# Kernel tuning notes

Measured on AMD Instinct MI355X. Metric: run time of the kernel, lower is better.

The kernel has to match this reference:

```python
import jax, jax.numpy as jnp
import numpy as np

N_NODES, N_EDGES, D_IN, D_H, N_GRAPHS = 50000, 600000, 1024, 128, 1000


def _transformer_conv(x, src, dst, wq, bq, wk, bk, wv, bv, ws, bs, n):
    """PyG TransformerConv, heads=1, concat=True, root_weight=True."""
    q = x @ wq + bq                      # [N, d]
    k = x @ wk + bk
    v = x @ wv + bv
    d = q.shape[-1]
    # per-edge attention score for edge j->i: <q_i, k_j> / sqrt(d)
    score = jnp.sum(q[dst] * k[src], axis=-1) / jnp.sqrt(jnp.asarray(d, x.dtype))  # [E]
    # segment softmax over incoming edges of each destination node
    smax = jax.ops.segment_max(score, dst, num_segments=n)
    smax = jnp.where(jnp.isfinite(smax), smax, jnp.zeros_like(smax))
    ex = jnp.exp(score - smax[dst])
    denom = jax.ops.segment_sum(ex, dst, num_segments=n)
    alpha = ex / (denom[dst] + 1e-16)
    # scatter-aggregate weighted values back to destination nodes
    agg = jax.ops.segment_sum(alpha[:, None] * v[src], dst, num_segments=n)  # [N, d]
    # skip (root) connection
    return agg + x @ ws + bs


def setup_inputs() -> dict:
    key = jax.random.key(0)
    ks = jax.random.split(key, 20)
    inp = {}
    inp['x'] = jax.random.normal(ks[0], (N_NODES, D_IN), dtype=jnp.float32)
    inp['edge_index'] = jax.random.randint(ks[1], (2, N_EDGES), 0, N_NODES, dtype=jnp.int64)
    inp['idx'] = jax.random.randint(ks[2], (N_GRAPHS,), 0, N_NODES, dtype=jnp.int64)
    s_in = 0.02
    # layer 0: 1024 -> 128
    for i, nm in enumerate(['wq0', 'wk0', 'wv0', 'ws0']):
        inp[nm] = jax.random.normal(ks[3 + i], (D_IN, D_H), dtype=jnp.float32) * s_in
    for nm in ['bq0', 'bk0', 'bv0', 'bs0']:
        inp[nm] = jnp.zeros((D_H,), dtype=jnp.float32)
    # layer 1: 128 -> 128
    for i, nm in enumerate(['wq1', 'wk1', 'wv1', 'ws1']):
        inp[nm] = jax.random.normal(ks[7 + i], (D_H, D_H), dtype=jnp.float32) * 0.08
    for nm in ['bq1', 'bk1', 'bv1', 'bs1']:
        inp[nm] = jnp.zeros((D_H,), dtype=jnp.float32)
    # MLP head 128 -> 128 -> 64 -> 1
    inp['mw1'] = jax.random.normal(ks[11], (D_H, D_H), dtype=jnp.float32) * 0.08
    inp['mb1'] = jnp.zeros((D_H,), dtype=jnp.float32)
    inp['mw2'] = jax.random.normal(ks[12], (D_H, 64), dtype=jnp.float32) * 0.08
    inp['mb2'] = jnp.zeros((64,), dtype=jnp.float32)
    inp['mw3'] = jax.random.normal(ks[13], (64, 1), dtype=jnp.float32) * 0.1
    inp['mb3'] = jnp.zeros((1,), dtype=jnp.float32)
    return inp


def reference(x, edge_index, idx,
              wq0, bq0, wk0, bk0, wv0, bv0, ws0, bs0,
              wq1, bq1, wk1, bk1, wv1, bv1, ws1, bs1,
              mw1, mb1, mw2, mb2, mw3, mb3):
    src, dst = edge_index[0], edge_index[1]
    n = x.shape[0]
    h = _transformer_conv(x, src, dst, wq0, bq0, wk0, bk0, wv0, bv0, ws0, bs0, n)
    h = jax.nn.relu(h)
    h = _transformer_conv(h, src, dst, wq1, bq1, wk1, bk1, wv1, bv1, ws1, bs1, n)
    h = jax.nn.relu(h)
    h = h[idx]                           # one center node per graph -> [B, d]
    h = jax.nn.relu(h @ mw1 + mb1)       # dropout is identity in eval
    h = jax.nn.relu(h @ mw2 + mb2)
    out = jax.nn.sigmoid(h @ mw3 + mb3)  # [B, 1]
    return out
```

## Files before the change

### kernel.cpp

```cpp
#include <hip/hip_runtime.h>
#include <hip/hip_bf16.h>
#include <cstdint>
#include <cstddef>

typedef __bf16 bf16x2 __attribute__((ext_vector_type(2)));
typedef __bf16 bf16x8 __attribute__((ext_vector_type(8)));
typedef float f32x4 __attribute__((ext_vector_type(4)));

__device__ __forceinline__ void gl_lds16(const __bf16* g, __bf16* l) {
    __builtin_amdgcn_global_load_lds(
        (const __attribute__((address_space(1))) unsigned int*)g,
        (__attribute__((address_space(3))) unsigned int*)l, 16, 0, 0);
}

template <typename AT> struct ARaw;
template <> struct ARaw<float>  { float4 u, v; };
template <> struct ARaw<__bf16> { bf16x8 w; };

template <typename AT>
__device__ __forceinline__ void loadAraw(const AT* p, ARaw<AT>& r) {
    if constexpr (sizeof(AT) == 4) {
        r.u = *(const float4*)p;
        r.v = *(const float4*)(p + 4);
    } else {
        r.w = *(const bf16x8*)p;
    }
}

template <typename AT>
__device__ __forceinline__ bf16x8 cvtA(const ARaw<AT>& r) {
    if constexpr (sizeof(AT) == 4) {
        return (bf16x8){(__bf16)r.u.x, (__bf16)r.u.y, (__bf16)r.u.z, (__bf16)r.u.w,
                        (__bf16)r.v.x, (__bf16)r.v.y, (__bf16)r.v.z, (__bf16)r.v.w};
    } else {
        return r.w;
    }
}

__global__ __launch_bounds__(256) void mark_idx_kernel(const int* __restrict__ idx,
                                                       int* __restrict__ flagIdx,
                                                       int* __restrict__ flagU, int B) {
    int t = blockIdx.x * 256 + threadIdx.x;
    if (t < B) {
        int n = idx[t];
        flagIdx[n] = 1;
        flagU[n] = 1;
    }
}

__global__ __launch_bounds__(256) void hist_mark_kernel(const int* __restrict__ esrc,
                                                        const int* __restrict__ edst,
                                                        const int* __restrict__ flagIdx,
                                                        int* __restrict__ deg,
                                                        int* __restrict__ flagU, int E) {
    int e = blockIdx.x * 256 + threadIdx.x;
    if (e < E) {
        int d = edst[e];
        atomicAdd(&deg[d], 1);
        if (flagIdx[d]) flagU[esrc[e]] = 1;
    }
}

__global__ __launch_bounds__(1024) void scan8_kernel(const int* __restrict__ deg,
                                                     int* __restrict__ off, int n,
                                                     const int* __restrict__ flagU,
                                                     int* __restrict__ U,
                                                     int* __restrict__ nU) {
    __shared__ int wsum[16];
    int tid = threadIdx.x, lane = tid & 63, wid = tid >> 6;
    if (tid == 0) off[0] = 0;
    int carry = 0;
    int nchunk = (n + 8191) >> 13;
    for (int c = 0; c < nchunk; ++c) {
        int base = (c << 13) + tid * 8;
        int4 a = *(const int4*)(deg + base);
        int4 b = *(const int4*)(deg + base + 4);
        int s[8];
        s[0] = a.x; s[1] = s[0] + a.y; s[2] = s[1] + a.z; s[3] = s[2] + a.w;
        s[4] = s[3] + b.x; s[5] = s[4] + b.y; s[6] = s[5] + b.z; s[7] = s[6] + b.w;
        int x = s[7];
        for (int o = 1; o < 64; o <<= 1) {
            int t = __shfl_up(x, o, 64);
            if (lane >= o) x += t;
        }
        if (lane == 63) wsum[wid] = x;
        __syncthreads();
        if (wid == 0 && lane < 16) {
            int w = wsum[lane];
            for (int o = 1; o < 16; o <<= 1) {
                int t = __shfl_up(w, o, 64);
                if (lane >= o) w += t;
            }
            wsum[lane] = w;
        }
        __syncthreads();
        int pre = carry + (wid ? wsum[wid - 1] : 0) + (x - s[7]);
#pragma unroll
        for (int i = 0; i < 8; ++i)
            if (base + i < n) off[base + i + 1] = pre + s[i];
        carry += wsum[15];
        __syncthreads();
    }
    for (int i = tid; i < n; i += 1024)
        if (flagU[i]) U[atomicAdd(nU, 1)] = i;
}

__global__ __launch_bounds__(256) void scatter_kernel(const int* __restrict__ src,
                                                      const int* __restrict__ dst,
                                                      const int* __restrict__ off,
                                                      int* __restrict__ cursor,
                                                      int* __restrict__ srcs, int E) {
    int e = blockIdx.x * 256 + threadIdx.x;
    if (e < E) {
        int d = dst[e];
        int p = off[d] + atomicAdd(&cursor[d], 1);
        srcs[p] = src[e];
    }
}

__global__ __launch_bounds__(256) void pack_w_kernel(const float* __restrict__ wq0, const float* __restrict__ wk0,
                                                     const float* __restrict__ wv0, const float* __restrict__ ws0,
                                                     const float* __restrict__ wq1, const float* __restrict__ wk1,
                                                     const float* __restrict__ wv1, const float* __restrict__ ws1,
                                                     const float* __restrict__ bq0, const float* __restrict__ bk0,
                                                     const float* __restrict__ bv0, const float* __restrict__ bs0,
                                                     const float* __restrict__ bq1, const float* __restrict__ bk1,
                                                     const float* __restrict__ bv1, const float* __restrict__ bs1,
                                                     __bf16* __restrict__ w0t, __bf16* __restrict__ w1t,
                                                     float* __restrict__ b0, float* __restrict__ b1) {
    int i = blockIdx.x * 256 + threadIdx.x;
    const int S0 = 512 * 1024, S1 = 512 * 128;
    if (i < S0) {
        int n = i >> 10, k = i & 1023;
        int sel = n >> 7, c = n & 127;
        const float* w = (sel == 0) ? wk0 : (sel == 1) ? wv0 : (sel == 2) ? wq0 : ws0;
        w0t[i] = (__bf16)w[(size_t)k * 128 + c];
    } else if (i < S0 + S1) {
        int j = i - S0;
        int n = j >> 7, k = j & 127;
        int sel = n >> 7, c = n & 127;
        const float* w = (sel == 0) ? wk1 : (sel == 1) ? wv1 : (sel == 2) ? wq1 : ws1;
        w1t[j] = (__bf16)w[(size_t)k * 128 + c];
    } else if (i < S0 + S1 + 512) {
        int t = i - S0 - S1;
        int sel = t >> 7, c = t & 127;
        const float* b = (sel == 0) ? bk0 : (sel == 1) ? bv0 : (sel == 2) ? bq0 : bs0;
        b0[t] = b[c];
    } else if (i < S0 + S1 + 1024) {
        int t = i - S0 - S1 - 512;
        int sel = t >> 7, c = t & 127;
        const float* b = (sel == 0) ? bk1 : (sel == 1) ? bv1 : (sel == 2) ? bq1 : bs1;
        b1[t] = b[c];
    }
}

template <typename AT>
__global__ __launch_bounds__(512, 4) void gemm_dual_kernel(const AT* __restrict__ A,
                                                           const __bf16* __restrict__ Bt,
                                                           const float* __restrict__ bias,
                                                           __bf16* __restrict__ outb,
                                                           float* __restrict__ outf,
                                                           const int* __restrict__ rl0,
                                                           const int* __restrict__ np0, int ns0,
                                                           const int* __restrict__ rl1,
                                                           const int* __restrict__ np1, int ns1,
                                                           int K, int s0blocks) {
    __shared__ __align__(16) __bf16 Asl[2][128 * 32];
    __shared__ __align__(16) __bf16 Bsl[3][256 * 32];
    const int bx = blockIdx.x;
    const int sector = (bx >= s0blocks) ? 1 : 0;
    const int tile0  = sector ? bx - s0blocks : bx;
    const int tstr   = sector ? (gridDim.x - s0blocks) : s0blocks;
    const int* rowlist = sector ? rl1 : rl0;
    const int* nptr = sector ? np1 : np0;
    const int nrows = nptr ? *nptr : (sector ? ns1 : ns0);
    if (nrows <= 0) return;
    const __bf16* BT = Bt + (size_t)(sector ? 256 : 0) * K;
    const float* bs = bias + (sector ? 256 : 0);
    const int ntiles = (nrows + 127) >> 7;
    const int NT = K >> 5;

    const int tid = threadIdx.x;
    const int lane = tid & 63, wid = tid >> 6;
    const int wm = wid >> 2, wn = wid & 3;
    const int fr = lane & 15, quad = lane >> 4;
    const int rr = tid >> 2;
    const int kc8 = (tid & 3) << 3;
    const int swch = (((tid & 3) ^ (rr & 3)) << 3);
    const int qsw8 = ((quad ^ (fr & 3)) << 3);

    const __bf16* gB = BT + (size_t)rr * K + swch;

    for (int mt = tile0; mt < ntiles; mt += tstr) {
        const int mbase = mt << 7;
        int lr = mbase + rr;
        if (lr >= nrows) lr = nrows - 1;
        const int gr = rowlist ? rowlist[lr] : lr;
        const AT* gA = A + (size_t)gr * K + kc8;

        f32x4 acc[4][4];
#pragma unroll
        for (int i = 0; i < 4; i++)
#pragma unroll
            for (int j = 0; j < 4; j++) acc[i][j] = (f32x4){0.f, 0.f, 0.f, 0.f};

        __syncthreads();

        ARaw<AT> a0, aC;
        {
            __bf16* bd0 = &Bsl[0][(size_t)(wid << 4) * 32];
            gl_lds16(gB, bd0);
            gl_lds16(gB + (size_t)128 * K, bd0 + 128 * 32);
            loadAraw(gA, a0);
            __bf16* bd1 = &Bsl[1][(size_t)(wid << 4) * 32];
            gl_lds16(gB + 32, bd1);
            gl_lds16(gB + (size_t)128 * K + 32, bd1 + 128 * 32);
            loadAraw(gA + 32, aC);
            *(bf16x8*)&Asl[0][rr * 32 + swch] = cvtA<AT>(a0);
            asm volatile("s_waitcnt lgkmcnt(0)" ::: "memory");
            __builtin_amdgcn_s_barrier();
        }

        for (int k = 0; k < NT; ++k) {
            const __bf16* As = Asl[k & 1];
            const __bf16* Bs = Bsl[k % 3];
            bf16x8 af[4];
#pragma unroll
            for (int mi = 0; mi < 4; mi++)
                af[mi] = *(const bf16x8*)&As[(wm * 64 + mi * 16 + fr) * 32 + qsw8];
#pragma unroll
            for (int ni = 0; ni < 4; ni++) {
                bf16x8 b8 = *(const bf16x8*)&Bs[(wn * 64 + ni * 16 + fr) * 32 + qsw8];
#pragma unroll
                for (int mi = 0; mi < 4; mi++)
                    acc[mi][ni] = __builtin_amdgcn_mfma_f32_16x16x32_bf16(af[mi], b8, acc[mi][ni], 0, 0, 0);
            }
            const bool wr = (k + 1 < NT);
            const bool pf = (k + 2 < NT);
            if (pf) {
                const int kn = (k + 2) << 5;
                __bf16* bd = &Bsl[(k + 2) % 3][(size_t)(wid << 4) * 32];
                gl_lds16(gB + kn, bd);
                gl_lds16(gB + (size_t)128 * K + kn, bd + 128 * 32);
            }
            if (wr) {
                *(bf16x8*)&Asl[(k + 1) & 1][rr * 32 + swch] = cvtA<AT>(aC);
            }
            if (pf) {
                loadAraw(gA + ((k + 2) << 5), aC);
            }
            if (wr) {
                asm volatile("s_waitcnt lgkmcnt(0)" ::: "memory");
                __builtin_amdgcn_s_barrier();
            }
        }

#pragma unroll
        for (int mi = 0; mi < 4; mi++)
#pragma unroll
            for (int ni = 0; ni < 4; ni++) {
                int rl = wm * 64 + mi * 16 + quad * 4;
                int cl = wn * 64 + ni * 16 + fr;
                float b = bs[cl];
#pragma unroll
                for (int r = 0; r < 4; r++) {
                    int lr2 = mbase + rl + r;
                    if (lr2 < nrows) {
                        int gr2 = rowlist ? rowlist[lr2] : lr2;
                        float v = acc[mi][ni][r] + b;
                        if (sector == 0) outb[(size_t)gr2 * 256 + cl] = (__bf16)v;
                        else             outf[(size_t)gr2 * 256 + cl] = v;
                    }
                }
            }
    }
}

__global__ __launch_bounds__(256) void attn_kernel(const float* __restrict__ qs,
                                                   const __bf16* __restrict__ kvb,
                                                   const int* __restrict__ off,
                                                   const int* __restrict__ srcs,
                                                   const int* __restrict__ nodelist,
                                                   const int* __restrict__ nptr, int nstatic,
                                                   __bf16* __restrict__ outb,
                                                   float* __restrict__ outf, int mode) {
    int n = nptr ? *nptr : nstatic;
    int lane = threadIdx.x & 63;
    int w0 = blockIdx.x * 4 + (threadIdx.x >> 6);
    int nw = gridDim.x * 4;
    const float scale = 0.08838834764831845f;
    for (int w = w0; w < n; w += nw) {
        int node = nodelist ? nodelist[w] : w;
        const float* bq = qs + (size_t)node * 256;
        float2 q = *(const float2*)(bq + 2 * lane);
        float2 s = *(const float2*)(bq + 128 + 2 * lane);
        int e0 = off[node], e1 = off[node + 1];
        float m = -INFINITY, l = 0.f;
        float ax = 0.f, ay = 0.f;
        bf16x2 kc = {(__bf16)0.f, (__bf16)0.f}, vc = kc;
        if (e0 < e1) {
            const __bf16* p = kvb + (size_t)srcs[e0] * 256;
            kc = *(const bf16x2*)(p + 2 * lane);
            vc = *(const bf16x2*)(p + 128 + 2 * lane);
        }
        for (int e = e0; e < e1; ++e) {
            bf16x2 kn = {(__bf16)0.f, (__bf16)0.f}, vn = kn;
            if (e + 1 < e1) {
                const __bf16* p = kvb + (size_t)srcs[e + 1] * 256;
                kn = *(const bf16x2*)(p + 2 * lane);
                vn = *(const bf16x2*)(p + 128 + 2 * lane);
            }
            float t = q.x * (float)kc.x + q.y * (float)kc.y;
#pragma unroll
            for (int o = 32; o > 0; o >>= 1) t += __shfl_xor(t, o, 64);
            float sc = t * scale;
            float mn = fmaxf(m, sc);
            float al = __expf(m - mn);
            float ee = __expf(sc - mn);
            ax = ax * al + ee * (float)vc.x;
            ay = ay * al + ee * (float)vc.y;
            l = l * al + ee;
            m = mn;
            kc = kn; vc = vn;
        }
        float inv = 1.f / (l + 1e-16f);
        float ox = ax * inv + s.x, oy = ay * inv + s.y;
        if (mode) {
            bf16x2 o2 = {(__bf16)fmaxf(ox, 0.f), (__bf16)fmaxf(oy, 0.f)};
            *(bf16x2*)(outb + (size_t)node * 128 + 2 * lane) = o2;
        } else {
            float2 o2 = {fmaxf(ox, 0.f), fmaxf(oy, 0.f)};
            *(float2*)(outf + (size_t)w * 128 + 2 * lane) = o2;
        }
    }
}

__global__ __launch_bounds__(128) void mlp_kernel(const float* __restrict__ hbuf,
                                                  const float* __restrict__ mw1, const float* __restrict__ mb1,
                                                  const float* __restrict__ mw2, const float* __restrict__ mb2,
                                                  const float* __restrict__ mw3, const float* __restrict__ mb3,
                                                  float* __restrict__ out, int B) {
    int b = blockIdx.x;
    int t = threadIdx.x;
    if (b >= B) return;
    __shared__ float xr[128], z1[128], z2[64];
    xr[t] = hbuf[(size_t)b * 128 + t];
    __syncthreads();
    float a1 = mb1[t];
#pragma unroll 8
    for (int k = 0; k < 128; ++k) a1 += xr[k] * mw1[k * 128 + t];
    z1[t] = fmaxf(a1, 0.f);
    __syncthreads();
    if (t < 64) {
        float a2 = mb2[t];
#pragma unroll 8
        for (int k = 0; k < 128; ++k) a2 += z1[k] * mw2[k * 64 + t];
        z2[t] = fmaxf(a2, 0.f);
    }
    __syncthreads();
    if (t < 64) {
        float p = z2[t] * mw3[t];
#pragma unroll
        for (int o = 32; o > 0; o >>= 1) p += __shfl_xor(p, o, 64);
        if (t == 0) out[b] = 1.f / (1.f + __expf(-(p + mb3[0])));
    }
}

extern "C" void kernel_launch(void* const* d_in, const int* in_sizes, int n_in,
                              void* d_out, int out_size, void* d_ws, size_t ws_size,
                              hipStream_t stream) {
    const float* x   = (const float*)d_in[0];
    const int*   ei  = (const int*)d_in[1];
    const int*   idx = (const int*)d_in[2];
    const float* wq0 = (const float*)d_in[3];
    const float* wk0 = (const float*)d_in[4];
    const float* wv0 = (const float*)d_in[5];
    const float* ws0 = (const float*)d_in[6];
    const float* bq0 = (const float*)d_in[7];
    const float* bk0 = (const float*)d_in[8];
    const float* bv0 = (const float*)d_in[9];
    const float* bs0 = (const float*)d_in[10];
    const float* wq1 = (const float*)d_in[11];
    const float* wk1 = (const float*)d_in[12];
    const float* wv1 = (const float*)d_in[13];
    const float* ws1 = (const float*)d_in[14];
    const float* bq1 = (const float*)d_in[15];
    const float* bk1 = (const float*)d_in[16];
    const float* bv1 = (const float*)d_in[17];
    const float* bs1 = (const float*)d_in[18];
    const float* mw1 = (const float*)d_in[19];
    const float* mb1 = (const float*)d_in[20];
    const float* mw2 = (const float*)d_in[21];
    const float* mb2 = (const float*)d_in[22];
    const float* mw3 = (const float*)d_in[23];
    const float* mb3 = (const float*)d_in[24];
    float* out = (float*)d_out;

    const int Nn = in_sizes[0] / 1024;
    const int E  = in_sizes[1] / 2;
    const int B  = in_sizes[2];
    const int* esrc = ei;
    const int* edst = ei + E;
    const int degPad = ((Nn + 8191) >> 13) << 13;

    uintptr_t base = (uintptr_t)d_ws;
    auto alloc = [&](size_t bytes) -> void* {
        uintptr_t p = (base + 255) & ~(uintptr_t)255;
        base = p + bytes;
        return (void*)p;
    };
    __bf16* kvb  = (__bf16*)alloc((size_t)Nn * 256 * 2);
    __bf16* kv1b = kvb;
    float*  qs   = (float*)alloc((size_t)Nn * 256 * 4);
    float*  qs1  = qs;
    __bf16* h0b  = (__bf16*)alloc((size_t)Nn * 128 * 2);
    float*  hbuf = (float*)alloc((size_t)B * 128 * 4);
    __bf16* w0t  = (__bf16*)alloc(512 * 1024 * 2);
    __bf16* w1t  = (__bf16*)alloc(512 * 128 * 2);
    float*  b0   = (float*)alloc(512 * 4);
    float*  b1   = (float*)alloc(512 * 4);
    int* deg     = (int*)alloc((size_t)degPad * 4);
    int* cursor  = (int*)alloc((size_t)Nn * 4);
    int* flagIdx = (int*)alloc((size_t)Nn * 4);
    int* flagU   = (int*)alloc((size_t)Nn * 4);
    int* nU      = (int*)alloc(256);
    size_t zbytes = (uintptr_t)nU + 256 - (uintptr_t)deg;
    int* off     = (int*)alloc((size_t)(Nn + 1) * 4);
    int* srcs    = (int*)alloc((size_t)E * 4);
    int* U       = (int*)alloc((size_t)Nn * 4);

    hipMemsetAsync(deg, 0, zbytes, stream);

    mark_idx_kernel<<<(B + 255) / 256, 256, 0, stream>>>(idx, flagIdx, flagU, B);
    hist_mark_kernel<<<(E + 255) / 256, 256, 0, stream>>>(esrc, edst, flagIdx, deg, flagU, E);
    scan8_kernel<<<1, 1024, 0, stream>>>(deg, off, Nn, flagU, U, nU);
    scatter_kernel<<<(E + 255) / 256, 256, 0, stream>>>(esrc, edst, off, cursor, srcs, E);

    pack_w_kernel<<<(512 * 1024 + 512 * 128 + 1024 + 255) / 256, 256, 0, stream>>>(
        wq0, wk0, wv0, ws0, wq1, wk1, wv1, ws1,
        bq0, bk0, bv0, bs0, bq1, bk1, bv1, bs1, w0t, w1t, b0, b1);

    const int mtiles = (Nn + 127) / 128;

    gemm_dual_kernel<float><<<mtiles + 121, 512, 0, stream>>>(x, w0t, b0, kvb, qs,
                                                              nullptr, nullptr, Nn,
                                                              U, nU, 0, 1024, mtiles);
    attn_kernel<<<4096, 256, 0, stream>>>(qs, kvb, off, srcs, U, nU, 0, h0b, nullptr, 1);

    gemm_dual_kernel<__bf16><<<144, 512, 0, stream>>>(h0b, w1t, b1, kv1b, qs1,
                                                      U, nU, 0,
                                                      idx, nullptr, B, 128, 128);
    attn_kernel<<<(B + 3) / 4, 256, 0, stream>>>(qs1, kv1b, off, srcs, idx, nullptr, B, nullptr, hbuf, 0);

    mlp_kernel<<<B, 128, 0, stream>>>(hbuf, mw1, mb1, mw2, mb2, mw3, mb3, out, B);
}
```

Before: 572.3 us.

## Load A fragments directly into registers, bypassing LDS staging in GEMM

The GEMM kernel stops staging the A tile through shared memory. Each wave now loads its own MFMA A fragments straight from global memory into registers, converting and prefetching them two k-steps ahead. Synchronisation moves from lgkmcnt waits to vmcnt-based waits, and launch bounds drop from 4 to 2 blocks per CU to give the extra register buffers room. This removes LDS writes and reads for A, but each A element is now loaded by four waves (one per wn), which raises global and L2 traffic and lowers occupancy.

```diff
diff --git a/kernel.cpp b/kernel.cpp
--- a/kernel.cpp
+++ b/kernel.cpp
@@ -155,7 +155,7 @@
 }
 
 template <typename AT>
-__global__ __launch_bounds__(512, 4) void gemm_dual_kernel(const AT* __restrict__ A,
+__global__ __launch_bounds__(512, 2) void gemm_dual_kernel(const AT* __restrict__ A,
                                                            const __bf16* __restrict__ Bt,
                                                            const float* __restrict__ bias,
                                                            __bf16* __restrict__ outb,
@@ -165,7 +165,6 @@
                                                            const int* __restrict__ rl1,
                                                            const int* __restrict__ np1, int ns1,
                                                            int K, int s0blocks) {
-    __shared__ __align__(16) __bf16 Asl[2][128 * 32];
     __shared__ __align__(16) __bf16 Bsl[3][256 * 32];
     const int bx = blockIdx.x;
     const int sector = (bx >= s0blocks) ? 1 : 0;
@@ -185,18 +184,48 @@
     const int wm = wid >> 2, wn = wid & 3;
     const int fr = lane & 15, quad = lane >> 4;
     const int rr = tid >> 2;
-    const int kc8 = (tid & 3) << 3;
     const int swch = (((tid & 3) ^ (rr & 3)) << 3);
     const int qsw8 = ((quad ^ (fr & 3)) << 3);
 
     const __bf16* gB = BT + (size_t)rr * K + swch;
 
+#define GSTEP(kk, afc, afn)                                                                   \
+    {                                                                                         \
+        const __bf16* Bs = &Bsl[(kk) % 3][0];                                                 \
+        _Pragma("unroll")                                                                     \
+        for (int ni = 0; ni < 4; ni++) {                                                      \
+            bf16x8 b8 = *(const bf16x8*)&Bs[(wn * 64 + ni * 16 + fr) * 32 + qsw8];            \
+            _Pragma("unroll")                                                                 \
+            for (int mi = 0; mi < 4; mi++)                                                    \
+                acc[mi][ni] = __builtin_amdgcn_mfma_f32_16x16x32_bf16(afc[mi], b8,            \
+                                                                     acc[mi][ni], 0, 0, 0);   \
+        }                                                                                     \
+        _Pragma("unroll")                                                                     \
+        for (int mi = 0; mi < 4; mi++) afn[mi] = cvtA<AT>(rawA[mi]);                          \
+        const int kc = ((kk) + 2 < NT) ? (((kk) + 2) << 5) : ((NT - 1) << 5);                 \
+        _Pragma("unroll")                                                                     \
+        for (int mi = 0; mi < 4; mi++) loadAraw(aptr[mi] + kc, rawA[mi]);                     \
+        __bf16* bd = &Bsl[((kk) + 2) % 3][(size_t)(wid << 4) * 32];                           \
+        gl_lds16(gB + kc, bd);                                                                \
+        gl_lds16(gB + (size_t)128 * K + kc, bd + 128 * 32);                                   \
+        if constexpr (sizeof(AT) == 4)                                                        \
+            asm volatile("s_waitcnt vmcnt(10)" ::: "memory");                                 \
+        else                                                                                  \
+            asm volatile("s_waitcnt vmcnt(6)" ::: "memory");                                  \
+        __builtin_amdgcn_s_barrier();                                                         \
+    }
+
     for (int mt = tile0; mt < ntiles; mt += tstr) {
         const int mbase = mt << 7;
-        int lr = mbase + rr;
-        if (lr >= nrows) lr = nrows - 1;
-        const int gr = rowlist ? rowlist[lr] : lr;
-        const AT* gA = A + (size_t)gr * K + kc8;
+
+        const AT* aptr[4];
+#pragma unroll
+        for (int mi = 0; mi < 4; mi++) {
+            int lr2 = mbase + wm * 64 + mi * 16 + fr;
+            if (lr2 >= nrows) lr2 = nrows - 1;
+            int g2 = rowlist ? rowlist[lr2] : lr2;
+            aptr[mi] = A + (size_t)g2 * K + quad * 8;
+        }
 
         f32x4 acc[4][4];
 #pragma unroll
@@ -206,53 +235,32 @@
 
         __syncthreads();
 
-        ARaw<AT> a0, aC;
+        ARaw<AT> rawA[4];
+        bf16x8 afA[4], afB[4];
+
         {
+#pragma unroll
+            for (int mi = 0; mi < 4; mi++) loadAraw(aptr[mi], rawA[mi]);
             __bf16* bd0 = &Bsl[0][(size_t)(wid << 4) * 32];
             gl_lds16(gB, bd0);
             gl_lds16(gB + (size_t)128 * K, bd0 + 128 * 32);
-            loadAraw(gA, a0);
+#pragma unroll
+            for (int mi = 0; mi < 4; mi++) afA[mi] = cvtA<AT>(rawA[mi]);
+#pragma unroll
+            for (int mi = 0; mi < 4; mi++) loadAraw(aptr[mi] + 32, rawA[mi]);
             __bf16* bd1 = &Bsl[1][(size_t)(wid << 4) * 32];
             gl_lds16(gB + 32, bd1);
             gl_lds16(gB + (size_t)128 * K + 32, bd1 + 128 * 32);
-            loadAraw(gA + 32, aC);
-            *(bf16x8*)&Asl[0][rr * 32 + swch] = cvtA<AT>(a0);
-            asm volatile("s_waitcnt lgkmcnt(0)" ::: "memory");
+            if constexpr (sizeof(AT) == 4)
+                asm volatile("s_waitcnt vmcnt(10)" ::: "memory");
+            else
+                asm volatile("s_waitcnt vmcnt(6)" ::: "memory");
             __builtin_amdgcn_s_barrier();
         }
 
-        for (int k = 0; k < NT; ++k) {
-            const __bf16* As = Asl[k & 1];
-            const __bf16* Bs = Bsl[k % 3];
-            bf16x8 af[4];
-#pragma unroll
-            for (int mi = 0; mi < 4; mi++)
-                af[mi] = *(const bf16x8*)&As[(wm * 64 + mi * 16 + fr) * 32 + qsw8];
-#pragma unroll
-            for (int ni = 0; ni < 4; ni++) {
-                bf16x8 b8 = *(const bf16x8*)&Bs[(wn * 64 + ni * 16 + fr) * 32 + qsw8];
-#pragma unroll
-                for (int mi = 0; mi < 4; mi++)
-                    acc[mi][ni] = __builtin_amdgcn_mfma_f32_16x16x32_bf16(af[mi], b8, acc[mi][ni], 0, 0, 0);
-            }
-            const bool wr = (k + 1 < NT);
-            const bool pf = (k + 2 < NT);
-            if (pf) {
-                const int kn = (k + 2) << 5;
-                __bf16* bd = &Bsl[(k + 2) % 3][(size_t)(wid << 4) * 32];
-                gl_lds16(gB + kn, bd);
-                gl_lds16(gB + (size_t)128 * K + kn, bd + 128 * 32);
-            }
-            if (wr) {
-                *(bf16x8*)&Asl[(k + 1) & 1][rr * 32 + swch] = cvtA<AT>(aC);
-            }
-            if (pf) {
-                loadAraw(gA + ((k + 2) << 5), aC);
-            }
-            if (wr) {
-                asm volatile("s_waitcnt lgkmcnt(0)" ::: "memory");
-                __builtin_amdgcn_s_barrier();
-            }
+        for (int kk = 0; kk < NT; kk += 2) {
+            GSTEP(kk, afA, afB)
+            GSTEP(kk + 1, afB, afA)
         }
 
 #pragma unroll
@@ -274,6 +282,7 @@
                 }
             }
     }
+#undef GSTEP
 }
 
 __global__ __launch_bounds__(256) void attn_kernel(const float* __restrict__ qs,
```

Result: slower. 686.0 us (+19.9%).
